# Performance work log

Hardware: AMD Instinct MI355X
Metric: run time of the kernel (lower is better)

Reference implementation:

```python
import jax, jax.numpy as jnp
import numpy as np

B, T, C, H = 4, 2048, 1024, 16
D = C // H  # head dim = 64

def setup_inputs() -> dict:
    key = jax.random.key(0)
    k1, k2, k3 = jax.random.split(key, 3)
    x = jax.random.normal(k1, (B, T, C), dtype=jnp.float32)
    # torch Linear weight [out,in]; store transposed for x @ W
    W_attn = jax.random.normal(k2, (C, 3 * C), dtype=jnp.float32) * (1.0 / np.sqrt(C))
    W_proj = jax.random.normal(k3, (C, C), dtype=jnp.float32) * (1.0 / np.sqrt(C))
    return {"x": x, "W_attn": W_attn, "W_proj": W_proj}

def reference(x, W_attn, W_proj):
    qkv = x @ W_attn                          # [B,T,3C]
    q, k, v = jnp.split(qkv, 3, axis=-1)
    # [B,T,C] -> [B,H,T,D]
    def heads(t):
        return t.reshape(B, T, H, D).transpose(0, 2, 1, 3)
    q, k, v = heads(q), heads(k), heads(v)
    att = jnp.einsum('bhqd,bhkd->bhqk', q, k) * (1.0 / np.sqrt(D))  # [B,H,T,T]
    causal = jnp.tril(jnp.ones((T, T), dtype=bool))
    att = jnp.where(causal[None, None, :, :], att, -jnp.inf)
    att = jax.nn.softmax(att, axis=-1)
    y = jnp.einsum('bhqk,bhkd->bhqd', att, v)  # [B,H,T,D]
    y = y.transpose(0, 2, 1, 3).reshape(B, T, C)
    return y @ W_proj
```

## Files before the change

### kernel.cpp

```cpp
#include <hip/hip_runtime.h>
#include <hip/hip_bf16.h>

#define BB 4
#define TT 2048
#define CC 1024
#define HH 16
#define DD 64
#define MM (BB*TT)

typedef unsigned short u16;
typedef __bf16 bf16x8 __attribute__((ext_vector_type(8)));
typedef __bf16 bf16x4v __attribute__((ext_vector_type(4)));
typedef u16 u16x8 __attribute__((ext_vector_type(8)));
typedef u16 u16x4 __attribute__((ext_vector_type(4)));
typedef float f32x4 __attribute__((ext_vector_type(4)));

__device__ __forceinline__ u16 f2bf(float f) {
  union { float f; unsigned u; } v; v.f = f;
  unsigned u = v.u;
  return (u16)((u + 0x7fffu + ((u >> 16) & 1u)) >> 16);
}
__device__ __forceinline__ float bf2f(u16 s) {
  union { unsigned u; float f; } v; v.u = ((unsigned)s) << 16; return v.f;
}
__device__ __forceinline__ bf16x8 ld_bf16x8(const u16* p) {
  return *reinterpret_cast<const bf16x8*>(p);
}
__device__ __forceinline__ f32x4 zero4() {
  f32x4 z; z[0] = 0.f; z[1] = 0.f; z[2] = 0.f; z[3] = 0.f; return z;
}

__device__ __forceinline__ void gld_lds16(const u16* g, u16* l) {
  __builtin_amdgcn_global_load_lds(
      (const __attribute__((address_space(1))) void*)g,
      (__attribute__((address_space(3))) void*)l, 16, 0, 0);
}
__device__ __forceinline__ void wait_vm0() { __builtin_amdgcn_s_waitcnt(0x0F70); }

__device__ __forceinline__ float lane_pull(float x, int srclane) {
  int r = __builtin_amdgcn_ds_bpermute(srclane << 2, __builtin_bit_cast(int, x));
  return __builtin_bit_cast(float, r);
}

#define NC4B ((MM * CC / 4) / 256)
__global__ void k_prep(const float* __restrict__ x, u16* __restrict__ xb,
                       const float* __restrict__ Wa, u16* __restrict__ Wab,
                       const float* __restrict__ Wp, u16* __restrict__ Wpb) {
  __shared__ float tile[32][33];
  const int bx = blockIdx.x;
  if (bx < NC4B) {
    int i = bx * 256 + threadIdx.x;
    const float4 v = reinterpret_cast<const float4*>(x)[i];
    u16x4 r; r.x = f2bf(v.x); r.y = f2bf(v.y); r.z = f2bf(v.z); r.w = f2bf(v.w);
    reinterpret_cast<u16x4*>(xb)[i] = r;
    return;
  }
  const float* W; u16* Wt; int K, N, b2;
  if (bx < NC4B + 3072) { W = Wa; Wt = Wab; K = CC; N = 3 * CC; b2 = bx - NC4B; }
  else                  { W = Wp; Wt = Wpb; K = CC; N = CC;     b2 = bx - NC4B - 3072; }
  const int nblk = N / 32;
  const int nb = (b2 % nblk) * 32, kb = (b2 / nblk) * 32;
  const int tx = threadIdx.x & 31, ty = threadIdx.x >> 5;
  #pragma unroll
  for (int i = ty; i < 32; i += 8)
    tile[i][tx] = W[(size_t)(kb + i) * N + nb + tx];
  __syncthreads();
  #pragma unroll
  for (int i = ty; i < 32; i += 8)
    Wt[(size_t)(nb + i) * K + kb + tx] = f2bf(tile[tx][i]);
}

template<int EPI>
__global__ __launch_bounds__(256, 3)
void k_gemm_bt(const u16* __restrict__ A, const u16* __restrict__ Bt,
               float* __restrict__ outF, u16* __restrict__ qb, u16* __restrict__ kb,
               u16* __restrict__ vt, int N, int K)
{
  __shared__ u16 As[128 * 64];
  __shared__ u16 Bs[128 * 64];
  const int tid  = threadIdx.x;
  const int lane = tid & 63, w = tid >> 6;
  const int l16  = lane & 15, quad = lane >> 4;
  const int wr = w >> 1, wc = w & 1;
  const int m0 = blockIdx.y * 128, n0 = blockIdx.x * 128;
  const int lr8 = lane >> 3, lc8 = lane & 7;

  f32x4 acc[4][4];
  #pragma unroll
  for (int i = 0; i < 4; ++i)
    #pragma unroll
    for (int j = 0; j < 4; ++j) acc[i][j] = zero4();

  for (int k0 = 0; k0 < K; k0 += 64) {
    __syncthreads();
    #pragma unroll
    for (int p = 0; p < 4; ++p) {
      const int row = w * 32 + p * 8 + lr8;
      const int cs  = lc8 ^ (row & 7);
      gld_lds16(A  + (size_t)(m0 + row) * K + k0 + cs * 8, &As[(w * 32 + p * 8) * 64]);
      gld_lds16(Bt + (size_t)(n0 + row) * K + k0 + cs * 8, &Bs[(w * 32 + p * 8) * 64]);
    }
    wait_vm0();
    __syncthreads();
    #pragma unroll
    for (int s = 0; s < 2; ++s) {
      bf16x8 af[4], bfr[4];
      #pragma unroll
      for (int i = 0; i < 4; ++i) {
        int mrow = wr * 64 + i * 16 + l16;
        af[i]  = ld_bf16x8(&As[mrow * 64 + ((s * 4 + quad) ^ (l16 & 7)) * 8]);
        int nrow = wc * 64 + i * 16 + l16;
        bfr[i] = ld_bf16x8(&Bs[nrow * 64 + ((s * 4 + quad) ^ (l16 & 7)) * 8]);
      }
      #pragma unroll
      for (int i = 0; i < 4; ++i)
        #pragma unroll
        for (int j = 0; j < 4; ++j)
          acc[i][j] = __builtin_amdgcn_mfma_f32_16x16x32_bf16(af[i], bfr[j], acc[i][j], 0, 0, 0);
    }
  }

  #pragma unroll
  for (int i = 0; i < 4; ++i) {
    #pragma unroll
    for (int j = 0; j < 4; ++j) {
      const int n = n0 + wc * 64 + j * 16 + l16;
      const int mb = m0 + wr * 64 + i * 16 + quad * 4;
      if (EPI == 0) {
        #pragma unroll
        for (int r = 0; r < 4; ++r)
          outF[(size_t)(mb + r) * N + n] = acc[i][j][r];
      } else {
        const int b = mb >> 11, tb = mb & 2047;
        if (n < CC) {
          const int h = n >> 6, d = n & 63;
          #pragma unroll
          for (int r = 0; r < 4; ++r)
            qb[(((size_t)(b * HH + h) * TT + tb + r) << 6) + d] = f2bf(acc[i][j][r]);
        } else if (n < 2 * CC) {
          const int n2 = n - CC; const int h = n2 >> 6, d = n2 & 63;
          #pragma unroll
          for (int r = 0; r < 4; ++r)
            kb[(((size_t)(b * HH + h) * TT + tb + r) << 6) + d] = f2bf(acc[i][j][r]);
        } else {
          const int n2 = n - 2 * CC; const int h = n2 >> 6, d = n2 & 63;
          u16x4 cv;
          #pragma unroll
          for (int r = 0; r < 4; ++r) cv[r] = f2bf(acc[i][j][r]);
          *reinterpret_cast<u16x4*>(
              vt + ((size_t)(b * HH + h) * DD + d) * TT + tb) = cv;
        }
      }
    }
  }
}

__global__ __launch_bounds__(256, 3)
void k_attn(const u16* __restrict__ qb, const u16* __restrict__ kb,
            const u16* __restrict__ vt, u16* __restrict__ y)
{
  __shared__ u16 Ks[128 * 64];
  __shared__ u16 Vs[64 * 128];
  __shared__ u16 QP[8 * 1024];
  const int tid  = threadIdx.x;
  const int lane = tid & 63, w = tid >> 6;
  const int l16  = lane & 15, quad = lane >> 4;
  const int lr8 = lane >> 3, lc8 = lane & 7;

  const int bx = blockIdx.x;
  const int qt = 15 - (bx >> 6);
  const int bh = bx & 63;
  const int h  = bh & 15, b = bh >> 4;

  const u16* qptr = qb + ((size_t)bh * TT + qt * 128) * DD;
  const u16* kptr = kb + (size_t)bh * TT * DD;
  const u16* vptr = vt + (size_t)bh * DD * TT;

  const float qscale = 0.125f * 1.44269504088896340736f;
  #pragma unroll
  for (int p = 0; p < 4; ++p) {
    const int r = w * 32 + p * 8 + lr8;
    u16x8 v = *reinterpret_cast<const u16x8*>(qptr + (size_t)r * DD + lc8 * 8);
    u16x8 o;
    #pragma unroll
    for (int e = 0; e < 8; ++e) o[e] = f2bf(bf2f(v[e]) * qscale);
    *reinterpret_cast<u16x8*>(&Ks[r * 64 + (lc8 ^ lr8) * 8]) = o;
  }
  __syncthreads();
  bf16x8 qf0[2], qf1[2];
  #pragma unroll
  for (int s = 0; s < 2; ++s) {
    qf0[s] = ld_bf16x8(&Ks[(w * 16 + l16) * 64 + ((s * 4 + quad) ^ (l16 & 7)) * 8]);
    qf1[s] = ld_bf16x8(&Ks[(64 + w * 16 + l16) * 64 + ((s * 4 + quad) ^ (l16 & 7)) * 8]);
  }

  float rsum0 = 0.f, rsum1 = 0.f;
  f32x4 O0[4], O1[4];
  #pragma unroll
  for (int j = 0; j < 4; ++j) { O0[j] = zero4(); O1[j] = zero4(); }

  const int nkt = qt + 1;
  for (int kt = 0; kt < nkt; ++kt) {
    __syncthreads();
    {
      const u16* kt0 = kptr + (size_t)kt * 128 * DD;
      #pragma unroll
      for (int p = 0; p < 4; ++p) {
        const int row = w * 32 + p * 8 + lr8;
        const int cs  = lc8 ^ lr8;
        gld_lds16(kt0 + (size_t)row * DD + cs * 8, &Ks[(w * 32 + p * 8) * 64]);
      }
      #pragma unroll
      for (int p = 0; p < 4; ++p) {
        const int d  = w * 16 + p * 4 + (lane >> 4);
        const int cs = (lane & 15) ^ (d & 7);
        gld_lds16(vptr + (size_t)d * TT + kt * 128 + cs * 8,
                  &Vs[(w * 16 + p * 4) * 128]);
      }
    }
    wait_vm0();
    __syncthreads();

    #pragma unroll
    for (int h2 = 0; h2 < 2; ++h2) {
      const int  last = (kt == qt);
      const bool g0on = !(last && h2 == 1);
      f32x4 St0[4], St1[4];
      #pragma unroll
      for (int j = 0; j < 4; ++j) { St0[j] = zero4(); St1[j] = zero4(); }
      #pragma unroll
      for (int s = 0; s < 2; ++s) {
        bf16x8 kfr[4];
        #pragma unroll
        for (int j = 0; j < 4; ++j)
          kfr[j] = ld_bf16x8(&Ks[(h2 * 64 + j * 16 + l16) * 64 +
                                 ((s * 4 + quad) ^ (l16 & 7)) * 8]);
        if (g0on) {
          #pragma unroll
          for (int j = 0; j < 4; ++j)
            St0[j] = __builtin_amdgcn_mfma_f32_16x16x32_bf16(kfr[j], qf0[s], St0[j], 0, 0, 0);
        }
        #pragma unroll
        for (int j = 0; j < 4; ++j)
          St1[j] = __builtin_amdgcn_mfma_f32_16x16x32_bf16(kfr[j], qf1[s], St1[j], 0, 0, 0);
      }
      if (last) {
        const int qg = w * 16 + l16;
        if (h2 == 0) {
          #pragma unroll
          for (int j = 0; j < 4; ++j)
            #pragma unroll
            for (int r = 0; r < 4; ++r)
              if (j * 16 + quad * 4 + r > qg) St0[j][r] = -__builtin_inff();
        } else {
          #pragma unroll
          for (int j = 0; j < 4; ++j)
            #pragma unroll
            for (int r = 0; r < 4; ++r)
              if (j * 16 + quad * 4 + r > qg) St1[j][r] = -__builtin_inff();
        }
      }

      if (g0on) {
        #pragma unroll
        for (int j = 0; j < 4; ++j)
          #pragma unroll
          for (int r = 0; r < 4; ++r) {
            float p = __builtin_amdgcn_exp2f(St0[j][r]);
            St0[j][r] = p; rsum0 += p;
          }
        #pragma unroll
        for (int j = 0; j < 4; ++j) {
          union { bf16x4v bv; u16x4 u; } cv;
          cv.bv[0] = (__bf16)St0[j][0]; cv.bv[1] = (__bf16)St0[j][1];
          cv.bv[2] = (__bf16)St0[j][2]; cv.bv[3] = (__bf16)St0[j][3];
          const int c = j * 2 + (quad >> 1);
          const int off = (w * 2 + 0) * 1024 + l16 * 64 +
                          ((c ^ (l16 & 7)) << 3) + ((quad & 1) << 2);
          *reinterpret_cast<u16x4*>(&QP[off]) = cv.u;
        }
      }
      #pragma unroll
      for (int j = 0; j < 4; ++j)
        #pragma unroll
        for (int r = 0; r < 4; ++r) {
          float p = __builtin_amdgcn_exp2f(St1[j][r]);
          St1[j][r] = p; rsum1 += p;
        }
      #pragma unroll
      for (int j = 0; j < 4; ++j) {
        union { bf16x4v bv; u16x4 u; } cv;
        cv.bv[0] = (__bf16)St1[j][0]; cv.bv[1] = (__bf16)St1[j][1];
        cv.bv[2] = (__bf16)St1[j][2]; cv.bv[3] = (__bf16)St1[j][3];
        const int c = j * 2 + (quad >> 1);
        const int off = (w * 2 + 1) * 1024 + l16 * 64 +
                        ((c ^ (l16 & 7)) << 3) + ((quad & 1) << 2);
        *reinterpret_cast<u16x4*>(&QP[off]) = cv.u;
      }

      #pragma unroll
      for (int s = 0; s < 2; ++s) {
        bf16x8 pf0, pf1;
        if (g0on)
          pf0 = ld_bf16x8(&QP[(w * 2 + 0) * 1024 + l16 * 64 +
                              ((s * 4 + quad) ^ (l16 & 7)) * 8]);
        pf1 = ld_bf16x8(&QP[(w * 2 + 1) * 1024 + l16 * 64 +
                            ((s * 4 + quad) ^ (l16 & 7)) * 8]);
        #pragma unroll
        for (int j = 0; j < 4; ++j) {
          bf16x8 vf = ld_bf16x8(&Vs[(j * 16 + l16) * 128 +
                                    ((h2 * 8 + s * 4 + quad) ^ (l16 & 7)) * 8]);
          if (g0on)
            O0[j] = __builtin_amdgcn_mfma_f32_16x16x32_bf16(pf0, vf, O0[j], 0, 0, 0);
          O1[j] = __builtin_amdgcn_mfma_f32_16x16x32_bf16(pf1, vf, O1[j], 0, 0, 0);
        }
      }
    }
  }

  #pragma unroll
  for (int g = 0; g < 2; ++g) {
    float rs = (g == 0) ? rsum0 : rsum1;
    rs += __shfl_xor(rs, 16);
    rs += __shfl_xor(rs, 32);
    const float linv = 1.0f / rs;
    f32x4 lv;
    #pragma unroll
    for (int r = 0; r < 4; ++r) lv[r] = lane_pull(linv, quad * 4 + r);
    #pragma unroll
    for (int j = 0; j < 4; ++j) {
      f32x4 o = (g == 0) ? O0[j] : O1[j];
      o *= lv;
      #pragma unroll
      for (int r = 0; r < 4; ++r) {
        int t  = qt * 128 + g * 64 + w * 16 + quad * 4 + r;
        int ch = h * 64 + j * 16 + l16;
        y[(size_t)(b * TT + t) * CC + ch] = f2bf(o[r]);
      }
    }
  }
}

extern "C" void kernel_launch(void* const* d_in, const int* in_sizes, int n_in,
                              void* d_out, int out_size, void* d_ws, size_t ws_size,
                              hipStream_t stream) {
  const float* x  = (const float*)d_in[0];
  const float* Wa = (const float*)d_in[1];
  const float* Wp = (const float*)d_in[2];
  float* out = (float*)d_out;

  u16* ws   = (u16*)d_ws;
  u16* xb   = ws;
  u16* Wab  = xb   + (size_t)MM * CC;
  u16* Wpb  = Wab  + (size_t)3 * CC * CC;
  u16* qbuf = Wpb  + (size_t)CC * CC;
  u16* kbuf = qbuf + (size_t)MM * CC;
  u16* vtb  = kbuf + (size_t)MM * CC;
  u16* yb   = vtb  + (size_t)MM * CC;

  k_prep<<<NC4B + 3072 + 1024, 256, 0, stream>>>(x, xb, Wa, Wab, Wp, Wpb);
  k_gemm_bt<1><<<dim3(3 * CC / 128, MM / 128), 256, 0, stream>>>(
      xb, Wab, nullptr, qbuf, kbuf, vtb, 3 * CC, CC);
  k_attn<<<64 * 16, 256, 0, stream>>>(qbuf, kbuf, vtb, yb);
  k_gemm_bt<0><<<dim3(CC / 128, MM / 128), 256, 0, stream>>>(
      yb, Wpb, out, nullptr, nullptr, nullptr, CC, CC);
}
```

Baseline: 214.9 us.

## Add 256x256-tile QKV GEMM with quarter-staged double buffering

Replaces the 128x128-tile QKV projection GEMM with a new 512-thread kernel that computes 256x256 output tiles. Operands are double-buffered in LDS using direct global-to-LDS loads, and the next K-slice is issued in quarters interleaved with the MFMA work, using partial vmcnt waits. The kernel also uses s_setprio around the MFMA blocks and a grouped block-index remap for L2 locality. The larger tiles raise arithmetic intensity and cut redundant operand loads, at the cost of 128 KB of LDS per block, more registers, and only 384 blocks, which limits occupancy and raises the risk of tail imbalance.

```diff
diff --git a/kernel.cpp b/kernel.cpp
--- a/kernel.cpp
+++ b/kernel.cpp
@@ -36,6 +36,8 @@
       (__attribute__((address_space(3))) void*)l, 16, 0, 0);
 }
 __device__ __forceinline__ void wait_vm0() { __builtin_amdgcn_s_waitcnt(0x0F70); }
+__device__ __forceinline__ void wait_vm2() { __builtin_amdgcn_s_waitcnt(0x0F72); }
+__device__ __forceinline__ void wait_vm4() { __builtin_amdgcn_s_waitcnt(0x0F74); }
 
 __device__ __forceinline__ float lane_pull(float x, int srclane) {
   int r = __builtin_amdgcn_ds_bpermute(srclane << 2, __builtin_bit_cast(int, x));
@@ -155,6 +157,125 @@
   }
 }
 
+__device__ __forceinline__ void stage_half256(const u16* __restrict__ G, u16* lbase,
+                                              int grow0, int kk, int lr8, int lc8) {
+  const int cs = (lc8 ^ lr8) << 3;
+  gld_lds16(G + (size_t)(grow0 + lr8) * CC + kk + cs, lbase);
+  gld_lds16(G + (size_t)(grow0 + 8 + lr8) * CC + kk + cs, lbase + 8 * 64);
+}
+
+__global__ __launch_bounds__(512, 2)
+void k_gemm256(const u16* __restrict__ A, const u16* __restrict__ Bt,
+               u16* __restrict__ qb, u16* __restrict__ kbuf, u16* __restrict__ vt)
+{
+  __shared__ u16 As[2][256 * 64];
+  __shared__ u16 Bs[2][256 * 64];
+  const int tid  = threadIdx.x;
+  const int lane = tid & 63, w = tid >> 6;
+  const int l16  = lane & 15, quad = lane >> 4;
+  const int lr8  = lane >> 3, lc8 = lane & 7;
+  const int wm = w >> 2, wn = w & 3;
+
+  const int lin = blockIdx.x;
+  const int nl  = (lin & 7) * 48 + (lin >> 3);
+  const int mt  = nl / 12, nt_ = nl % 12;
+  const int m0 = mt * 256, n0 = nt_ * 256;
+
+  f32x4 acc[4][4][2];
+  #pragma unroll
+  for (int q = 0; q < 4; ++q)
+    #pragma unroll
+    for (int i = 0; i < 4; ++i)
+      #pragma unroll
+      for (int j = 0; j < 2; ++j) acc[q][i][j] = zero4();
+
+  stage_half256(A,  &As[0][(0 * 128 + w * 16) * 64], m0 +       w * 16, 0, lr8, lc8);
+  stage_half256(Bt, &Bs[0][(0 * 128 + w * 16) * 64], n0 +       w * 16, 0, lr8, lc8);
+  stage_half256(Bt, &Bs[0][(1 * 128 + w * 16) * 64], n0 + 128 + w * 16, 0, lr8, lc8);
+  stage_half256(A,  &As[0][(1 * 128 + w * 16) * 64], m0 + 128 + w * 16, 0, lr8, lc8);
+  wait_vm4();
+  __builtin_amdgcn_s_barrier();
+
+  for (int t = 0; t < 16; ++t) {
+    const int bb = t & 1;
+    const bool notlast = (t < 15);
+    const int kk = (t + 1) << 6;
+    #pragma unroll
+    for (int q = 0; q < 4; ++q) {
+      const int qm = (q >> 1);
+      const int qn = (q == 1 || q == 2);
+      bf16x8 af[2][4], bfr[2][2];
+      #pragma unroll
+      for (int s = 0; s < 2; ++s) {
+        const int cs = ((s * 4 + quad) ^ (l16 & 7)) << 3;
+        #pragma unroll
+        for (int i = 0; i < 4; ++i)
+          af[s][i] = ld_bf16x8(&As[bb][(qm * 128 + wm * 64 + i * 16 + l16) * 64 + cs]);
+        #pragma unroll
+        for (int j = 0; j < 2; ++j)
+          bfr[s][j] = ld_bf16x8(&Bs[bb][(qn * 128 + wn * 32 + j * 16 + l16) * 64 + cs]);
+      }
+      if (notlast) {
+        if (q == 0)
+          stage_half256(A,  &As[bb ^ 1][(0 * 128 + w * 16) * 64], m0 +       w * 16, kk, lr8, lc8);
+        else if (q == 1)
+          stage_half256(Bt, &Bs[bb ^ 1][(0 * 128 + w * 16) * 64], n0 +       w * 16, kk, lr8, lc8);
+        else if (q == 2)
+          stage_half256(Bt, &Bs[bb ^ 1][(1 * 128 + w * 16) * 64], n0 + 128 + w * 16, kk, lr8, lc8);
+        else
+          stage_half256(A,  &As[bb ^ 1][(1 * 128 + w * 16) * 64], m0 + 128 + w * 16, kk, lr8, lc8);
+      }
+      __builtin_amdgcn_s_setprio(1);
+      #pragma unroll
+      for (int s = 0; s < 2; ++s)
+        #pragma unroll
+        for (int i = 0; i < 4; ++i)
+          #pragma unroll
+          for (int j = 0; j < 2; ++j)
+            acc[q][i][j] = __builtin_amdgcn_mfma_f32_16x16x32_bf16(
+                af[s][i], bfr[s][j], acc[q][i][j], 0, 0, 0);
+      __builtin_amdgcn_s_setprio(0);
+      if (notlast)       wait_vm4();
+      else if (q == 0)   wait_vm2();
+      else if (q == 1)   wait_vm0();
+      __builtin_amdgcn_s_barrier();
+    }
+  }
+
+  #pragma unroll
+  for (int q = 0; q < 4; ++q) {
+    const int qm = (q >> 1);
+    const int qn = (q == 1 || q == 2);
+    #pragma unroll
+    for (int i = 0; i < 4; ++i) {
+      #pragma unroll
+      for (int j = 0; j < 2; ++j) {
+        const int n  = n0 + qn * 128 + wn * 32 + j * 16 + l16;
+        const int mb = m0 + qm * 128 + wm * 64 + i * 16 + quad * 4;
+        const int b = mb >> 11, tb = mb & 2047;
+        if (n < CC) {
+          const int h = n >> 6, d = n & 63;
+          #pragma unroll
+          for (int r = 0; r < 4; ++r)
+            qb[(((size_t)(b * HH + h) * TT + tb + r) << 6) + d] = f2bf(acc[q][i][j][r]);
+        } else if (n < 2 * CC) {
+          const int n2 = n - CC; const int h = n2 >> 6, d = n2 & 63;
+          #pragma unroll
+          for (int r = 0; r < 4; ++r)
+            kbuf[(((size_t)(b * HH + h) * TT + tb + r) << 6) + d] = f2bf(acc[q][i][j][r]);
+        } else {
+          const int n2 = n - 2 * CC; const int h = n2 >> 6, d = n2 & 63;
+          u16x4 cv;
+          #pragma unroll
+          for (int r = 0; r < 4; ++r) cv[r] = f2bf(acc[q][i][j][r]);
+          *reinterpret_cast<u16x4*>(
+              vt + ((size_t)(b * HH + h) * DD + d) * TT + tb) = cv;
+        }
+      }
+    }
+  }
+}
+
 __global__ __launch_bounds__(256, 3)
 void k_attn(const u16* __restrict__ qb, const u16* __restrict__ kb,
             const u16* __restrict__ vt, u16* __restrict__ y)
@@ -359,8 +480,7 @@
   u16* yb   = vtb  + (size_t)MM * CC;
 
   k_prep<<<NC4B + 3072 + 1024, 256, 0, stream>>>(x, xb, Wa, Wab, Wp, Wpb);
-  k_gemm_bt<1><<<dim3(3 * CC / 128, MM / 128), 256, 0, stream>>>(
-      xb, Wab, nullptr, qbuf, kbuf, vtb, 3 * CC, CC);
+  k_gemm256<<<384, 512, 0, stream>>>(xb, Wab, qbuf, kbuf, vtb);
   k_attn<<<64 * 16, 256, 0, stream>>>(qbuf, kbuf, vtb, yb);
   k_gemm_bt<0><<<dim3(CC / 128, MM / 128), 256, 0, stream>>>(
       yb, Wpb, out, nullptr, nullptr, nullptr, CC, CC);
```

Result: slower. 245.9 us (+14.4%).

## Add 256x192-tile double-buffered QKV GEMM kernel with swizzled block order

Applied to the files above, without the earlier changes.

Replaces the 128x128-tile QKV projection GEMM with a new kernel that uses 256x192 output tiles, 512 threads, and double-buffered LDS loads that overlap the next K-slice fetch with MFMA work. Blocks are remapped so that consecutive blocks share A rows, which is meant to improve L2 reuse. The larger tile cuts global and LDS traffic per FLOP and gives exactly 512 blocks for the 3072x8192 output. In exchange it needs much more LDS (about 112KB) and many more accumulator registers, which limits occupancy.

```diff
diff --git a/kernel.cpp b/kernel.cpp
--- a/kernel.cpp
+++ b/kernel.cpp
@@ -155,6 +155,105 @@
   }
 }
 
+__global__ __launch_bounds__(512, 2)
+void k_gemm256(const u16* __restrict__ A, const u16* __restrict__ Bt,
+               u16* __restrict__ qb, u16* __restrict__ kbuf, u16* __restrict__ vt)
+{
+  __shared__ u16 As[2][256 * 64];
+  __shared__ u16 Bs[2][192 * 64];
+  const int tid  = threadIdx.x;
+  const int lane = tid & 63, w = tid >> 6;
+  const int l16  = lane & 15, quad = lane >> 4;
+  const int lr8  = lane >> 3, lc8 = lane & 7;
+  const int wm = w >> 2, wn = w & 3;
+
+  const int lin = blockIdx.x;
+  const int nl  = (lin & 7) * 64 + (lin >> 3);
+  const int mt  = nl >> 4, nt_ = nl & 15;
+  const int m0 = mt * 256, n0 = nt_ * 192;
+
+  f32x4 acc[8][3];
+  #pragma unroll
+  for (int i = 0; i < 8; ++i)
+    #pragma unroll
+    for (int j = 0; j < 3; ++j) acc[i][j] = zero4();
+
+  const int srow = w * 8 + lr8;
+  const int scs  = (lc8 ^ lr8) << 3;
+  const u16* Ab0 = A  + (size_t)(m0 + srow) * CC + scs;
+  const u16* Bb0 = Bt + (size_t)(n0 + srow) * CC + scs;
+
+  #pragma unroll
+  for (int p = 0; p < 4; ++p)
+    gld_lds16(Ab0 + (size_t)p * 64 * CC, &As[0][(p * 64 + w * 8) * 64]);
+  #pragma unroll
+  for (int p = 0; p < 3; ++p)
+    gld_lds16(Bb0 + (size_t)p * 64 * CC, &Bs[0][(p * 64 + w * 8) * 64]);
+  wait_vm0();
+  __builtin_amdgcn_s_barrier();
+
+  for (int t = 0; t < 16; ++t) {
+    const int bb = t & 1;
+    if (t < 15) {
+      const int kk = (t + 1) << 6;
+      #pragma unroll
+      for (int p = 0; p < 4; ++p)
+        gld_lds16(Ab0 + kk + (size_t)p * 64 * CC, &As[bb ^ 1][(p * 64 + w * 8) * 64]);
+      #pragma unroll
+      for (int p = 0; p < 3; ++p)
+        gld_lds16(Bb0 + kk + (size_t)p * 64 * CC, &Bs[bb ^ 1][(p * 64 + w * 8) * 64]);
+    }
+    #pragma unroll
+    for (int s = 0; s < 2; ++s) {
+      const int cs = ((s * 4 + quad) ^ (l16 & 7)) << 3;
+      bf16x8 af[8], bfr[3];
+      #pragma unroll
+      for (int i = 0; i < 8; ++i)
+        af[i] = ld_bf16x8(&As[bb][(wm * 128 + i * 16 + l16) * 64 + cs]);
+      #pragma unroll
+      for (int j = 0; j < 3; ++j)
+        bfr[j] = ld_bf16x8(&Bs[bb][(wn * 48 + j * 16 + l16) * 64 + cs]);
+      __builtin_amdgcn_s_setprio(1);
+      #pragma unroll
+      for (int i = 0; i < 8; ++i)
+        #pragma unroll
+        for (int j = 0; j < 3; ++j)
+          acc[i][j] = __builtin_amdgcn_mfma_f32_16x16x32_bf16(af[i], bfr[j], acc[i][j], 0, 0, 0);
+      __builtin_amdgcn_s_setprio(0);
+    }
+    wait_vm0();
+    __builtin_amdgcn_s_barrier();
+  }
+
+  #pragma unroll
+  for (int i = 0; i < 8; ++i) {
+    #pragma unroll
+    for (int j = 0; j < 3; ++j) {
+      const int n  = n0 + wn * 48 + j * 16 + l16;
+      const int mb = m0 + wm * 128 + i * 16 + quad * 4;
+      const int b = mb >> 11, tb = mb & 2047;
+      if (n < CC) {
+        const int h = n >> 6, d = n & 63;
+        #pragma unroll
+        for (int r = 0; r < 4; ++r)
+          qb[(((size_t)(b * HH + h) * TT + tb + r) << 6) + d] = f2bf(acc[i][j][r]);
+      } else if (n < 2 * CC) {
+        const int n2 = n - CC; const int h = n2 >> 6, d = n2 & 63;
+        #pragma unroll
+        for (int r = 0; r < 4; ++r)
+          kbuf[(((size_t)(b * HH + h) * TT + tb + r) << 6) + d] = f2bf(acc[i][j][r]);
+      } else {
+        const int n2 = n - 2 * CC; const int h = n2 >> 6, d = n2 & 63;
+        u16x4 cv;
+        #pragma unroll
+        for (int r = 0; r < 4; ++r) cv[r] = f2bf(acc[i][j][r]);
+        *reinterpret_cast<u16x4*>(
+            vt + ((size_t)(b * HH + h) * DD + d) * TT + tb) = cv;
+      }
+    }
+  }
+}
+
 __global__ __launch_bounds__(256, 3)
 void k_attn(const u16* __restrict__ qb, const u16* __restrict__ kb,
             const u16* __restrict__ vt, u16* __restrict__ y)
@@ -359,8 +458,7 @@
   u16* yb   = vtb  + (size_t)MM * CC;
 
   k_prep<<<NC4B + 3072 + 1024, 256, 0, stream>>>(x, xb, Wa, Wab, Wp, Wpb);
-  k_gemm_bt<1><<<dim3(3 * CC / 128, MM / 128), 256, 0, stream>>>(
-      xb, Wab, nullptr, qbuf, kbuf, vtb, 3 * CC, CC);
+  k_gemm256<<<512, 512, 0, stream>>>(xb, Wab, qbuf, kbuf, vtb);
   k_attn<<<64 * 16, 256, 0, stream>>>(qbuf, kbuf, vtb, yb);
   k_gemm_bt<0><<<dim3(CC / 128, MM / 128), 256, 0, stream>>>(
       yb, Wpb, out, nullptr, nullptr, nullptr, CC, CC);
```

Measured after the change: 229.7 us. 1.07x slower.
